# Kernel tuning notes

Hardware: AMD Instinct MI355X
Metric: run time of the kernel (lower is better)

Reference implementation:

```python
import jax, jax.numpy as jnp
import numpy as np

B = 100          # number of graphs in the batch
NODES_PER_GRAPH = 500
N_TOTAL = B * NODES_PER_GRAPH
T_MAX = 32
F_DIM = 128


def setup_inputs() -> dict:
    key = jax.random.key(0)
    k1, k2, k3 = jax.random.split(key, 3)
    nodes_output = jax.random.normal(k1, (N_TOTAL, T_MAX, F_DIM), dtype=jnp.float32)
    # valid temporal lengths in [1, T_MAX]
    lengths = jax.random.randint(k2, (B,), 1, T_MAX + 1, dtype=jnp.int64)
    num_nodes = jnp.full((B,), NODES_PER_GRAPH, dtype=jnp.int64)  # graph.batch_num_nodes()
    wq = jax.random.normal(k3, (F_DIM,), dtype=jnp.float32) * (1.0 / np.sqrt(F_DIM))
    return {"nodes_output": nodes_output, "lengths": lengths,
            "num_nodes": num_nodes, "wq": wq}


def reference(nodes_output, lengths, num_nodes, wq):
    # nodes_output: (N, T, F); wq: (F,) == nn.Linear(F,1,bias=False).weight
    N, T, _ = nodes_output.shape
    # unnormalized temporal scores per node/timestep: (N, T)
    scores = jnp.einsum('ntf,f->nt', nodes_output, wq)
    # broadcast each graph's length to its nodes: (N,)
    node_len = jnp.repeat(lengths, num_nodes, total_repeat_length=N)
    # mask out timesteps >= length (equivalent to slicing :length per graph)
    mask = jnp.arange(T)[None, :] < node_len[:, None]
    w = jnp.where(mask, scores, jnp.zeros((), dtype=scores.dtype))
    # weighted temporal sum: (N, F)
    return jnp.einsum('nt,ntf->nf', w, nodes_output)
```

## Files before the change

kernel.cpp:

```cpp
#include <hip/hip_runtime.h>

constexpr int TMAX = 32;
constexpr int FDIM = 128;

__global__ void prefix_kernel(const int* __restrict__ num_nodes, int* __restrict__ prefix, int B) {
    if (threadIdx.x == 0 && blockIdx.x == 0) {
        int acc = 0;
        for (int g = 0; g < B; ++g) {
            prefix[g] = acc;
            acc += num_nodes[g];
        }
        prefix[B] = acc;
    }
}

__global__ __launch_bounds__(256)
void aggregate_nodes_temporal_kernel(const float* __restrict__ x,
                                     const int* __restrict__ lengths,
                                     const int* __restrict__ prefix,
                                     const float* __restrict__ wq,
                                     float* __restrict__ out,
                                     int N, int B) {
    const int lane = threadIdx.x & 63;
    const int wid = threadIdx.x >> 6;
    const int n = blockIdx.x * 4 + wid;
    if (n >= N) return;

    int cnt = 0;
    for (int base = 0; base <= B; base += 64) {
        const int i = base + lane;
        const bool ok = (i <= B) && (prefix[i] <= n);
        cnt += __popcll(__ballot(ok));
    }
    const int g = cnt - 1;
    int len = lengths[g];
    if (len < 0) len = 0;
    if (len > TMAX) len = TMAX;

    const float2 wqv = reinterpret_cast<const float2*>(wq)[lane];
    const float2* src = reinterpret_cast<const float2*>(x) + (size_t)n * (TMAX * (FDIM / 2)) + lane;

    float2 row[TMAX];
#pragma unroll
    for (int t = 0; t < TMAX; ++t) {
        if (t < len) row[t] = src[t * (FDIM / 2)];
    }

    float2 acc = make_float2(0.0f, 0.0f);
#pragma unroll
    for (int t = 0; t < TMAX; ++t) {
        if (t < len) {
            float p = row[t].x * wqv.x + row[t].y * wqv.y;
#pragma unroll
            for (int off = 32; off >= 1; off >>= 1)
                p += __shfl_xor(p, off, 64);
            acc.x += p * row[t].x;
            acc.y += p * row[t].y;
        }
    }

    reinterpret_cast<float2*>(out)[(size_t)n * (FDIM / 2) + lane] = acc;
}

extern "C" void kernel_launch(void* const* d_in, const int* in_sizes, int n_in,
                              void* d_out, int out_size, void* d_ws, size_t ws_size,
                              hipStream_t stream) {
    const float* x = (const float*)d_in[0];
    const int* lengths = (const int*)d_in[1];
    const int* num_nodes = (const int*)d_in[2];
    const float* wq = (const float*)d_in[3];
    float* out = (float*)d_out;

    const int N = in_sizes[0] / (TMAX * FDIM);
    const int B = in_sizes[1];

    int* prefix = (int*)d_ws;

    prefix_kernel<<<1, 64, 0, stream>>>(num_nodes, prefix, B);
    const int blocks = (N + 3) / 4;
    aggregate_nodes_temporal_kernel<<<blocks, 256, 0, stream>>>(x, lengths, prefix, wq, out, N, B);
}
```

Baseline: 103.7 us.

## Fuse prefix scan into main kernel and use float4 loads over half-waves

```diff
diff --git a/kernel.cpp b/kernel.cpp
--- a/kernel.cpp
+++ b/kernel.cpp
@@ -3,21 +3,10 @@
 constexpr int TMAX = 32;
 constexpr int FDIM = 128;
 
-__global__ void prefix_kernel(const int* __restrict__ num_nodes, int* __restrict__ prefix, int B) {
-    if (threadIdx.x == 0 && blockIdx.x == 0) {
-        int acc = 0;
-        for (int g = 0; g < B; ++g) {
-            prefix[g] = acc;
-            acc += num_nodes[g];
-        }
-        prefix[B] = acc;
-    }
-}
-
 __global__ __launch_bounds__(256)
 void aggregate_nodes_temporal_kernel(const float* __restrict__ x,
                                      const int* __restrict__ lengths,
-                                     const int* __restrict__ prefix,
+                                     const int* __restrict__ num_nodes,
                                      const float* __restrict__ wq,
                                      float* __restrict__ out,
                                      int N, int B) {
@@ -27,39 +16,60 @@
     if (n >= N) return;
 
     int cnt = 0;
-    for (int base = 0; base <= B; base += 64) {
-        const int i = base + lane;
-        const bool ok = (i <= B) && (prefix[i] <= n);
-        cnt += __popcll(__ballot(ok));
+    int carry = 0;
+    for (int base = 0; base < B; base += 64) {
+        int v = (base + lane < B) ? num_nodes[base + lane] : 0;
+#pragma unroll
+        for (int off = 1; off < 64; off <<= 1) {
+            int u = __shfl_up(v, off, 64);
+            v += (lane >= off) ? u : 0;
+        }
+        const int incl = v + carry;
+        cnt += __popcll(__ballot(incl <= n));
+        carry = __shfl(incl, 63, 64);
     }
-    const int g = cnt - 1;
+    const int g = cnt;
+
     int len = lengths[g];
     if (len < 0) len = 0;
     if (len > TMAX) len = TMAX;
 
-    const float2 wqv = reinterpret_cast<const float2*>(wq)[lane];
-    const float2* src = reinterpret_cast<const float2*>(x) + (size_t)n * (TMAX * (FDIM / 2)) + lane;
+    const int half = lane >> 5;
+    const int fl = lane & 31;
+    const float4 wq4 = reinterpret_cast<const float4*>(wq)[fl];
+    const float4* src = reinterpret_cast<const float4*>(x)
+                      + (size_t)n * (TMAX * (FDIM / 4)) + half * (FDIM / 4) + fl;
 
-    float2 row[TMAX];
+    float4 row[TMAX / 2];
 #pragma unroll
-    for (int t = 0; t < TMAX; ++t) {
-        if (t < len) row[t] = src[t * (FDIM / 2)];
+    for (int k = 0; k < TMAX / 2; ++k) {
+        row[k] = make_float4(0.0f, 0.0f, 0.0f, 0.0f);
+        if (2 * k + half < len)
+            row[k] = src[k * (2 * FDIM / 4)];
     }
 
-    float2 acc = make_float2(0.0f, 0.0f);
+    float4 acc = make_float4(0.0f, 0.0f, 0.0f, 0.0f);
 #pragma unroll
-    for (int t = 0; t < TMAX; ++t) {
-        if (t < len) {
-            float p = row[t].x * wqv.x + row[t].y * wqv.y;
+    for (int k = 0; k < TMAX / 2; ++k) {
+        if (2 * k < len) {
+            float p = row[k].x * wq4.x + row[k].y * wq4.y
+                    + row[k].z * wq4.z + row[k].w * wq4.w;
 #pragma unroll
-            for (int off = 32; off >= 1; off >>= 1)
+            for (int off = 1; off < 32; off <<= 1)
                 p += __shfl_xor(p, off, 64);
-            acc.x += p * row[t].x;
-            acc.y += p * row[t].y;
+            acc.x += p * row[k].x;
+            acc.y += p * row[k].y;
+            acc.z += p * row[k].z;
+            acc.w += p * row[k].w;
         }
     }
 
-    reinterpret_cast<float2*>(out)[(size_t)n * (FDIM / 2) + lane] = acc;
+    acc.x += __shfl_xor(acc.x, 32, 64);
+    acc.y += __shfl_xor(acc.y, 32, 64);
+    acc.z += __shfl_xor(acc.z, 32, 64);
+    acc.w += __shfl_xor(acc.w, 32, 64);
+    if (half == 0)
+        reinterpret_cast<float4*>(out)[(size_t)n * (FDIM / 4) + fl] = acc;
 }
 
 extern "C" void kernel_launch(void* const* d_in, const int* in_sizes, int n_in,
@@ -74,9 +84,6 @@
     const int N = in_sizes[0] / (TMAX * FDIM);
     const int B = in_sizes[1];
 
-    int* prefix = (int*)d_ws;
-
-    prefix_kernel<<<1, 64, 0, stream>>>(num_nodes, prefix, B);
     const int blocks = (N + 3) / 4;
-    aggregate_nodes_temporal_kernel<<<blocks, 256, 0, stream>>>(x, lengths, prefix, wq, out, N, B);
+    aggregate_nodes_temporal_kernel<<<blocks, 256, 0, stream>>>(x, lengths, num_nodes, wq, out, N, B);
 }
```

Result: faster. 88.54 us (-14.6%).
